# Optimization experiments

Measured on AMD Instinct MI355X. Metric: run time of the kernel, lower is better.

Reference implementation:

```python
import jax, jax.numpy as jnp
import numpy as np

OUTPUT_DIM = 1024  # init kwarg output_dim


def _adaptive_avg_pool_last(x, out_dim):
    """Faithful F.adaptive_avg_pool1d over the last axis (static shapes)."""
    in_dim = x.shape[-1]
    if in_dim % out_dim == 0:
        k = in_dim // out_dim
        return x.reshape(x.shape[:-1] + (out_dim, k)).mean(axis=-1)
    # generic case: window i covers [floor(i*In/Out), ceil((i+1)*In/Out))
    idx = np.arange(out_dim)
    starts = (idx * in_dim) // out_dim
    ends = -((-(idx + 1) * in_dim) // out_dim)
    W = np.zeros((in_dim, out_dim), dtype=np.float32)
    for i in range(out_dim):
        W[starts[i]:ends[i], i] = 1.0 / (ends[i] - starts[i])
    return x @ jnp.asarray(W)


def _per_layer_gram(feat, output_dim):
    N, C, ph, pw = feat.shape
    P = ph * pw
    c_red = min(C, 64)
    f = feat.reshape(N, C, P).transpose(0, 2, 1)        # [N, P, C]
    f = _adaptive_avg_pool_last(f, c_red)               # [N, P, Cr] channel reduction
    fr = f.transpose(0, 2, 1)                           # [N, Cr, P]
    gram = jnp.einsum('ncp,ndp->ncd', fr, fr) / P       # [N, Cr, Cr] per-patch Gram
    return _adaptive_avg_pool_last(gram.reshape(N, c_red * c_red), output_dim)  # [N, output_dim]


def setup_inputs() -> dict:
    key = jax.random.key(0)
    k0, k1 = jax.random.split(key)
    feat0 = jax.random.normal(k0, (6272, 512, 3, 3), dtype=jnp.float32)
    feat1 = jax.random.normal(k1, (6272, 1024, 3, 3), dtype=jnp.float32)
    return {"feat0": feat0, "feat1": feat1}


def reference(feat0, feat1):
    # stack over layers -> [N, L=2, output_dim]
    return jnp.stack(
        [_per_layer_gram(feat0, OUTPUT_DIM), _per_layer_gram(feat1, OUTPUT_DIM)],
        axis=1,
    )
```

## Files before the change

kernel.cpp:

```cpp
#include <hip/hip_runtime.h>


#define N_SAMPLES 6272

__global__ __launch_bounds__(256, 8) void patchgram_kernel(
    const float* __restrict__ f0, const float* __restrict__ f1,
    float* __restrict__ out)
{
    __shared__ float4 fr4[64 * 3];
    __shared__ float4 B4[16 * 3];
    float* fr = (float*)fr4;
    float* B  = (float*)B4;

    const int bid   = blockIdx.x;
    const int n     = bid >> 1;
    const int layer = bid & 1;
    const int t     = threadIdx.x;

    const float* __restrict__ src = layer ? f1 : f0;
    const int nflt   = layer ? 9216 : 4608;
    const int nload  = nflt / 36;
    const int gshift = layer ? 2 : 1;

    if (t < nload) {
        const float4* __restrict__ g =
            (const float4*)(src + (size_t)n * nflt) + t * 9;
        float4 v[9];
#pragma unroll
        for (int j = 0; j < 9; ++j) v[j] = g[j];

        float acc[9];
#pragma unroll
        for (int p = 0; p < 9; ++p) acc[p] = 0.f;
#pragma unroll
        for (int j = 0; j < 9; ++j) {
            acc[(4 * j + 0) % 9] += v[j].x;
            acc[(4 * j + 1) % 9] += v[j].y;
            acc[(4 * j + 2) % 9] += v[j].z;
            acc[(4 * j + 3) % 9] += v[j].w;
        }
#pragma unroll
        for (int p = 0; p < 9; ++p) acc[p] += __shfl_xor(acc[p], 1);
        if (layer) {
#pragma unroll
            for (int p = 0; p < 9; ++p) acc[p] += __shfl_xor(acc[p], 2);
        }
        if ((t & ((1 << gshift) - 1)) == 0) {
            const int row = t >> gshift;
            fr4[row * 3 + 0] = make_float4(acc[0], acc[1], acc[2], acc[3]);
            fr4[row * 3 + 1] = make_float4(acc[4], acc[5], acc[6], acc[7]);
            fr4[row * 3 + 2] = make_float4(acc[8], 0.f, 0.f, 0.f);
        }
    }
    __syncthreads();

    if (t < 144) {
        const int dg = t / 9;
        const int p  = t - dg * 9;
        B[dg * 12 + p] = fr[(4 * dg + 0) * 12 + p] + fr[(4 * dg + 1) * 12 + p] +
                         fr[(4 * dg + 2) * 12 + p] + fr[(4 * dg + 3) * 12 + p];
    }
    __syncthreads();

    const int c   = t >> 2;
    const int dgq = t & 3;
    const float4 a0 = fr4[c * 3 + 0];
    const float4 a1 = fr4[c * 3 + 1];
    const float4 a2 = fr4[c * 3 + 2];
    const int   k     = layer ? 16 : 8;
    const float scale = 1.0f / (36.0f * (float)(k * k));

    float4 o4;
    float* op = (float*)&o4;
#pragma unroll
    for (int j = 0; j < 4; ++j) {
        const int d = dgq * 4 + j;
        const float4 b0 = B4[d * 3 + 0];
        const float4 b1 = B4[d * 3 + 1];
        const float4 b2 = B4[d * 3 + 2];
        float s = a0.x * b0.x + a0.y * b0.y + a0.z * b0.z + a0.w * b0.w
                + a1.x * b1.x + a1.y * b1.y + a1.z * b1.z + a1.w * b1.w
                + a2.x * b2.x;
        op[j] = s * scale;
    }
    float4* o = (float4*)(out + ((size_t)n * 2 + layer) * 1024 + c * 16 + dgq * 4);
    *o = o4;
}

extern "C" void kernel_launch(void* const* d_in, const int* in_sizes, int n_in,
                              void* d_out, int out_size, void* d_ws, size_t ws_size,
                              hipStream_t stream) {
    const float* f0 = (const float*)d_in[0];
    const float* f1 = (const float*)d_in[1];
    float* out = (float*)d_out;
    patchgram_kernel<<<N_SAMPLES * 2, 256, 0, stream>>>(f0, f1, out);
}
```

Before: 389.6 us.

## Stage per-sample features into LDS via coalesced async loads, split per-layer kernels

Each block now copies its whole sample's feature slice into shared memory with `global_load_lds` 16-byte transfers, indexed so consecutive threads read consecutive float4s. Previously each thread issued nine strided float4 loads straight into registers. The channel reduction then reads from shared memory. The single interleaved launch is replaced by two templated per-layer launches, which turns layer-dependent values into compile-time constants. The trade-off is a large LDS tile (up to 36 KB) that may reduce occupancy, plus an extra barrier and possible LDS bank conflicts on the stride-9 reads.

Measured after the change: 388.0 us. Within noise of the previous version (-0.4%).

```diff
diff --git a/kernel.cpp b/kernel.cpp
--- a/kernel.cpp
+++ b/kernel.cpp
@@ -3,50 +3,57 @@
 
 #define N_SAMPLES 6272
 
-__global__ __launch_bounds__(256, 8) void patchgram_kernel(
-    const float* __restrict__ f0, const float* __restrict__ f1,
-    float* __restrict__ out)
+typedef const __attribute__((address_space(1))) void* gas_ptr;
+typedef __attribute__((address_space(3))) void* las_ptr;
+
+__device__ __forceinline__ void load16_to_lds(const void* g, void* l) {
+    __builtin_amdgcn_global_load_lds((gas_ptr)g, (las_ptr)l, 16, 0, 0);
+}
+
+template <int CH>
+__global__ __launch_bounds__(256) void patchgram_layer(
+    const float* __restrict__ src, float* __restrict__ out)
 {
+    constexpr int NF   = CH * 9;
+    constexpr int NV4  = NF / 4;
+    constexpr int GSH  = (CH == 1024) ? 2 : 1;
+    constexpr int NRED = 64 << GSH;
+    constexpr int K    = CH / 64;
+    constexpr float SCALE = 1.0f / (36.0f * (float)(K * K));
+
+    __shared__ float4 tile[NV4];
     __shared__ float4 fr4[64 * 3];
     __shared__ float4 B4[16 * 3];
-    float* fr = (float*)fr4;
-    float* B  = (float*)B4;
 
-    const int bid   = blockIdx.x;
-    const int n     = bid >> 1;
-    const int layer = bid & 1;
-    const int t     = threadIdx.x;
+    const int n = blockIdx.x;
+    const int t = threadIdx.x;
 
-    const float* __restrict__ src = layer ? f1 : f0;
-    const int nflt   = layer ? 9216 : 4608;
-    const int nload  = nflt / 36;
-    const int gshift = layer ? 2 : 1;
+    const float4* __restrict__ g = (const float4*)(src + (size_t)n * NF);
+    for (int i = t; i < NV4; i += 256)
+        load16_to_lds(&g[i], &tile[i]);
+    __syncthreads();
 
-    if (t < nload) {
-        const float4* __restrict__ g =
-            (const float4*)(src + (size_t)n * nflt) + t * 9;
-        float4 v[9];
-#pragma unroll
-        for (int j = 0; j < 9; ++j) v[j] = g[j];
-
+    if (t < NRED) {
+        const float4* __restrict__ tp = &tile[t * 9];
         float acc[9];
 #pragma unroll
         for (int p = 0; p < 9; ++p) acc[p] = 0.f;
 #pragma unroll
         for (int j = 0; j < 9; ++j) {
-            acc[(4 * j + 0) % 9] += v[j].x;
-            acc[(4 * j + 1) % 9] += v[j].y;
-            acc[(4 * j + 2) % 9] += v[j].z;
-            acc[(4 * j + 3) % 9] += v[j].w;
+            const float4 v = tp[j];
+            acc[(4 * j + 0) % 9] += v.x;
+            acc[(4 * j + 1) % 9] += v.y;
+            acc[(4 * j + 2) % 9] += v.z;
+            acc[(4 * j + 3) % 9] += v.w;
         }
 #pragma unroll
         for (int p = 0; p < 9; ++p) acc[p] += __shfl_xor(acc[p], 1);
-        if (layer) {
+        if (GSH == 2) {
 #pragma unroll
             for (int p = 0; p < 9; ++p) acc[p] += __shfl_xor(acc[p], 2);
         }
-        if ((t & ((1 << gshift) - 1)) == 0) {
-            const int row = t >> gshift;
+        if ((t & ((1 << GSH) - 1)) == 0) {
+            const int row = t >> GSH;
             fr4[row * 3 + 0] = make_float4(acc[0], acc[1], acc[2], acc[3]);
             fr4[row * 3 + 1] = make_float4(acc[4], acc[5], acc[6], acc[7]);
             fr4[row * 3 + 2] = make_float4(acc[8], 0.f, 0.f, 0.f);
@@ -57,8 +64,10 @@
     if (t < 144) {
         const int dg = t / 9;
         const int p  = t - dg * 9;
-        B[dg * 12 + p] = fr[(4 * dg + 0) * 12 + p] + fr[(4 * dg + 1) * 12 + p] +
-                         fr[(4 * dg + 2) * 12 + p] + fr[(4 * dg + 3) * 12 + p];
+        const float* fr = (const float*)fr4;
+        ((float*)B4)[dg * 12 + p] =
+            fr[(4 * dg + 0) * 12 + p] + fr[(4 * dg + 1) * 12 + p] +
+            fr[(4 * dg + 2) * 12 + p] + fr[(4 * dg + 3) * 12 + p];
     }
     __syncthreads();
 
@@ -67,8 +76,6 @@
     const float4 a0 = fr4[c * 3 + 0];
     const float4 a1 = fr4[c * 3 + 1];
     const float4 a2 = fr4[c * 3 + 2];
-    const int   k     = layer ? 16 : 8;
-    const float scale = 1.0f / (36.0f * (float)(k * k));
 
     float4 o4;
     float* op = (float*)&o4;
@@ -81,9 +88,9 @@
         float s = a0.x * b0.x + a0.y * b0.y + a0.z * b0.z + a0.w * b0.w
                 + a1.x * b1.x + a1.y * b1.y + a1.z * b1.z + a1.w * b1.w
                 + a2.x * b2.x;
-        op[j] = s * scale;
+        op[j] = s * SCALE;
     }
-    float4* o = (float4*)(out + ((size_t)n * 2 + layer) * 1024 + c * 16 + dgq * 4);
+    float4* o = (float4*)(out + (size_t)n * 2048 + c * 16 + dgq * 4);
     *o = o4;
 }
 
@@ -93,5 +100,6 @@
     const float* f0 = (const float*)d_in[0];
     const float* f1 = (const float*)d_in[1];
     float* out = (float*)d_out;
-    patchgram_kernel<<<N_SAMPLES * 2, 256, 0, stream>>>(f0, f1, out);
+    patchgram_layer<512><<<N_SAMPLES, 256, 0, stream>>>(f0, out);
+    patchgram_layer<1024><<<N_SAMPLES, 256, 0, stream>>>(f1, out + 1024);
 }
```
